# Optimization experiments

Hardware: AMD Instinct MI355X
Metric: run time of the kernel (lower is better)

## Reference

```python
import jax, jax.numpy as jnp
import numpy as np

N_USER = 100000
N_ITEM = 50000
N_NODES = N_USER + N_ITEM
EMB = 64
NNZ = 4000000
BATCH = 4096
N_LAYERS = 3  # len(eval(args.layer_size)) with layer_size=[64,64,64]


def setup_inputs() -> dict:
    key = jax.random.key(0)
    k = jax.random.split(key, 8)
    adj_rows = jax.random.randint(k[0], (NNZ,), 0, N_NODES, dtype=jnp.int32)
    adj_cols = jax.random.randint(k[1], (NNZ,), 0, N_NODES, dtype=jnp.int32)
    adj_vals = jax.random.uniform(k[2], (NNZ,), dtype=jnp.float32)
    user_emb = jax.random.normal(k[3], (N_USER, EMB), dtype=jnp.float32)
    item_emb = jax.random.normal(k[4], (N_ITEM, EMB), dtype=jnp.float32)
    users = jax.random.randint(k[5], (BATCH,), 0, N_USER, dtype=jnp.int32)
    pos_items = jax.random.randint(k[6], (BATCH,), 0, N_ITEM, dtype=jnp.int32)
    neg_items = jax.random.randint(k[7], (BATCH,), 0, N_ITEM, dtype=jnp.int32)
    return {
        "adj_rows": adj_rows, "adj_cols": adj_cols, "adj_vals": adj_vals,
        "user_emb": user_emb, "item_emb": item_emb,
        "users": users, "pos_items": pos_items, "neg_items": neg_items,
    }


def _spmm(rows, cols, vals, x):
    # sparse [N,N] @ dense [N,D] via gather + segment-sum (COO)
    gathered = vals[:, None] * x[cols]          # [nnz, D]
    return jax.ops.segment_sum(gathered, rows, num_segments=N_NODES)


def reference(adj_rows, adj_cols, adj_vals, user_emb, item_emb,
              users, pos_items, neg_items):
    ego = jnp.concatenate([user_emb, item_emb], axis=0)  # [N, D]
    # Source quirk: ego_embeddings is never updated in the layer loop, so
    # every layer appends the same A_hat @ ego; mean over [ego] + L copies.
    prop = _spmm(adj_rows, adj_cols, adj_vals, ego)      # [N, D]
    light_out = (ego + N_LAYERS * prop) / (N_LAYERS + 1)
    u_g = light_out[:N_USER]
    i_g = light_out[N_USER:]
    out = jnp.stack([u_g[users], i_g[pos_items], i_g[neg_items]], axis=0)
    return out  # [3, BATCH, EMB]
```

## Files before the change

kernel.cpp:

```cpp
#include <hip/hip_runtime.h>

#define N_USER 100000
#define N_ITEM 50000
#define N_NODES 150000
#define EMB 64
#define NNZ 4000000
#define BATCH 4096
#define NSLOTS (3 * BATCH)
#define CAP 128

#define BM_OFF   0
#define CUR_OFF  19200
#define CT_OFF   68352
#define PROP_OFF 668416
#define BKT_OFF  3814144

__global__ void mark_kernel(const int* __restrict__ users,
                            const int* __restrict__ pos_items,
                            const int* __restrict__ neg_items,
                            unsigned int* __restrict__ bitmask,
                            int* __restrict__ ctab) {
    int t = blockIdx.x * blockDim.x + threadIdx.x;
    int k = t >> 12;
    int i = t & 4095;
    int node;
    if (k == 0)      node = users[i];
    else if (k == 1) node = N_USER + pos_items[i];
    else             node = N_USER + neg_items[i];
    atomicOr(bitmask + (node >> 5), 1u << (node & 31));
    atomicCAS(ctab + node, -1, t);
}

__global__ void scatter_kernel(const int* __restrict__ rows,
                               const int* __restrict__ cols,
                               const float* __restrict__ vals,
                               const unsigned int* __restrict__ bitmask,
                               const int* __restrict__ ctab,
                               unsigned int* __restrict__ cursor,
                               uint2* __restrict__ bucket) {
    int tid = blockIdx.x * blockDim.x + threadIdx.x;
    int row = rows[tid];
    int col = cols[tid];
    float val = vals[tid];
    unsigned int w = bitmask[row >> 5];
    if ((w >> (row & 31)) & 1) {
        int cid = ctab[row];
        unsigned int pos = atomicAdd(cursor + cid, 1u);
        if (pos < CAP)
            bucket[(size_t)cid * CAP + pos] =
                make_uint2((unsigned int)col, __float_as_uint(val));
    }
}

__global__ void accum_kernel(const unsigned int* __restrict__ cursor,
                             const uint2* __restrict__ bucket,
                             const float* __restrict__ user_emb,
                             const float* __restrict__ item_emb,
                             float* __restrict__ prop) {
    int t = blockIdx.x * blockDim.x + threadIdx.x;
    int wv = t >> 6;
    int lane = t & 63;
    unsigned int n = cursor[wv];
    if (n > CAP) n = CAP;
    const uint2* bkt = bucket + (size_t)wv * CAP;
    float acc = 0.0f;
    for (unsigned int base = 0; base < n; base += 8) {
        #pragma unroll
        for (int u = 0; u < 8; u++) {
            unsigned int e = base + (unsigned int)u;
            uint2 ev = bkt[e < n ? e : n - 1];
            int c = (int)ev.x;
            float v = __uint_as_float(ev.y);
            const float* x = (c < N_USER) ? user_emb + (size_t)c * EMB
                                          : item_emb + (size_t)(c - N_USER) * EMB;
            float xv = x[lane];
            acc += (e < n) ? v * xv : 0.0f;
        }
    }
    prop[(size_t)wv * EMB + lane] = acc;
}

__global__ void gather_kernel(const int* __restrict__ users,
                              const int* __restrict__ pos_items,
                              const int* __restrict__ neg_items,
                              const float* __restrict__ user_emb,
                              const float* __restrict__ item_emb,
                              const int* __restrict__ ctab,
                              const float* __restrict__ prop,
                              float* __restrict__ out) {
    int t = blockIdx.x * blockDim.x + threadIdx.x;
    int slot = t >> 4;
    int sub = t & 15;
    int k = slot >> 12;
    int i = slot & 4095;
    int node;
    if (k == 0)      node = users[i];
    else if (k == 1) node = N_USER + pos_items[i];
    else             node = N_USER + neg_items[i];
    const float4* ego = (const float4*)((node < N_USER)
                          ? user_emb + (size_t)node * EMB
                          : item_emb + (size_t)(node - N_USER) * EMB);
    float4 e = ego[sub];
    int cid = ctab[node];
    float4 p = ((const float4*)(prop + (size_t)cid * EMB))[sub];
    float4 o;
    o.x = (e.x + 3.0f * p.x) * 0.25f;
    o.y = (e.y + 3.0f * p.y) * 0.25f;
    o.z = (e.z + 3.0f * p.z) * 0.25f;
    o.w = (e.w + 3.0f * p.w) * 0.25f;
    ((float4*)out)[t] = o;
}

extern "C" void kernel_launch(void* const* d_in, const int* in_sizes, int n_in,
                              void* d_out, int out_size, void* d_ws, size_t ws_size,
                              hipStream_t stream) {
    const int*   adj_rows = (const int*)  d_in[0];
    const int*   adj_cols = (const int*)  d_in[1];
    const float* adj_vals = (const float*)d_in[2];
    const float* user_emb = (const float*)d_in[3];
    const float* item_emb = (const float*)d_in[4];
    const int*   users    = (const int*)  d_in[5];
    const int*   pos      = (const int*)  d_in[6];
    const int*   neg      = (const int*)  d_in[7];
    float* out = (float*)d_out;

    unsigned int* bitmask = (unsigned int*)((char*)d_ws + BM_OFF);
    unsigned int* cursor  = (unsigned int*)((char*)d_ws + CUR_OFF);
    int*          ctab    = (int*)         ((char*)d_ws + CT_OFF);
    float*        prop    = (float*)       ((char*)d_ws + PROP_OFF);
    uint2*        bucket  = (uint2*)       ((char*)d_ws + BKT_OFF);

    hipMemsetAsync((char*)d_ws + BM_OFF, 0, CT_OFF, stream);
    hipMemsetAsync((char*)d_ws + CT_OFF, 0xFF, N_NODES * 4, stream);

    mark_kernel<<<48, 256, 0, stream>>>(users, pos, neg, bitmask, ctab);

    scatter_kernel<<<15625, 256, 0, stream>>>(adj_rows, adj_cols, adj_vals,
                                              bitmask, ctab, cursor, bucket);

    accum_kernel<<<3072, 256, 0, stream>>>(cursor, bucket, user_emb, item_emb, prop);

    gather_kernel<<<768, 256, 0, stream>>>(users, pos, neg,
                                           user_emb, item_emb, ctab, prop, out);
}
```

Baseline: 171.8 us.

## Fuse accumulation into output gather, vectorize edge scan, drop ctab memset

The per-node accumulation is merged into the final gather kernel, so the intermediate prop buffer and one launch disappear. Each wave loads eight bucket entries cooperatively and broadcasts them with lane shuffles. The edge scatter now reads rows, cols and vals as 4-wide vectors, one thread per four edges. The ctab initialisation memset is removed by having mark_kernel do plain racing stores. In exchange, duplicate batch slots now each recompute their node's accumulation, and ctab entries for unmarked nodes keep stale values, which are never read.

Result: slower. 179.3 us (+4.4%).

```diff
diff --git a/kernel.cpp b/kernel.cpp
--- a/kernel.cpp
+++ b/kernel.cpp
@@ -12,8 +12,7 @@
 #define BM_OFF   0
 #define CUR_OFF  19200
 #define CT_OFF   68352
-#define PROP_OFF 668416
-#define BKT_OFF  3814144
+#define BKT_OFF  668416
 
 __global__ void mark_kernel(const int* __restrict__ users,
                             const int* __restrict__ pos_items,
@@ -28,87 +27,79 @@
     else if (k == 1) node = N_USER + pos_items[i];
     else             node = N_USER + neg_items[i];
     atomicOr(bitmask + (node >> 5), 1u << (node & 31));
-    atomicCAS(ctab + node, -1, t);
+    ctab[node] = t;
 }
 
-__global__ void scatter_kernel(const int* __restrict__ rows,
-                               const int* __restrict__ cols,
-                               const float* __restrict__ vals,
+#define E4 (NNZ / 4)
+__global__ void scatter_kernel(const int4* __restrict__ rows4,
+                               const int4* __restrict__ cols4,
+                               const float4* __restrict__ vals4,
                                const unsigned int* __restrict__ bitmask,
                                const int* __restrict__ ctab,
                                unsigned int* __restrict__ cursor,
                                uint2* __restrict__ bucket) {
-    int tid = blockIdx.x * blockDim.x + threadIdx.x;
-    int row = rows[tid];
-    int col = cols[tid];
-    float val = vals[tid];
-    unsigned int w = bitmask[row >> 5];
-    if ((w >> (row & 31)) & 1) {
-        int cid = ctab[row];
-        unsigned int pos = atomicAdd(cursor + cid, 1u);
-        if (pos < CAP)
-            bucket[(size_t)cid * CAP + pos] =
-                make_uint2((unsigned int)col, __float_as_uint(val));
+    int t = blockIdx.x * blockDim.x + threadIdx.x;
+    if (t >= E4) return;
+    int4   r4 = rows4[t];
+    int4   c4 = cols4[t];
+    float4 v4 = vals4[t];
+    int    rs[4] = {r4.x, r4.y, r4.z, r4.w};
+    int    cs[4] = {c4.x, c4.y, c4.z, c4.w};
+    float  vs[4] = {v4.x, v4.y, v4.z, v4.w};
+    #pragma unroll
+    for (int u = 0; u < 4; u++) {
+        int row = rs[u];
+        if ((bitmask[row >> 5] >> (row & 31)) & 1) {
+            int cid = ctab[row];
+            unsigned int pos = atomicAdd(cursor + cid, 1u);
+            if (pos < CAP)
+                bucket[(size_t)cid * CAP + pos] =
+                    make_uint2((unsigned int)cs[u], __float_as_uint(vs[u]));
+        }
     }
 }
 
-__global__ void accum_kernel(const unsigned int* __restrict__ cursor,
-                             const uint2* __restrict__ bucket,
-                             const float* __restrict__ user_emb,
-                             const float* __restrict__ item_emb,
-                             float* __restrict__ prop) {
+__global__ void accum_gather_kernel(const int* __restrict__ users,
+                                    const int* __restrict__ pos_items,
+                                    const int* __restrict__ neg_items,
+                                    const float* __restrict__ user_emb,
+                                    const float* __restrict__ item_emb,
+                                    const int* __restrict__ ctab,
+                                    const unsigned int* __restrict__ cursor,
+                                    const uint2* __restrict__ bucket,
+                                    float* __restrict__ out) {
     int t = blockIdx.x * blockDim.x + threadIdx.x;
-    int wv = t >> 6;
+    int slot = t >> 6;
     int lane = t & 63;
-    unsigned int n = cursor[wv];
-    if (n > CAP) n = CAP;
-    const uint2* bkt = bucket + (size_t)wv * CAP;
-    float acc = 0.0f;
-    for (unsigned int base = 0; base < n; base += 8) {
-        #pragma unroll
-        for (int u = 0; u < 8; u++) {
-            unsigned int e = base + (unsigned int)u;
-            uint2 ev = bkt[e < n ? e : n - 1];
-            int c = (int)ev.x;
-            float v = __uint_as_float(ev.y);
-            const float* x = (c < N_USER) ? user_emb + (size_t)c * EMB
-                                          : item_emb + (size_t)(c - N_USER) * EMB;
-            float xv = x[lane];
-            acc += (e < n) ? v * xv : 0.0f;
-        }
-    }
-    prop[(size_t)wv * EMB + lane] = acc;
-}
-
-__global__ void gather_kernel(const int* __restrict__ users,
-                              const int* __restrict__ pos_items,
-                              const int* __restrict__ neg_items,
-                              const float* __restrict__ user_emb,
-                              const float* __restrict__ item_emb,
-                              const int* __restrict__ ctab,
-                              const float* __restrict__ prop,
-                              float* __restrict__ out) {
-    int t = blockIdx.x * blockDim.x + threadIdx.x;
-    int slot = t >> 4;
-    int sub = t & 15;
     int k = slot >> 12;
     int i = slot & 4095;
     int node;
     if (k == 0)      node = users[i];
     else if (k == 1) node = N_USER + pos_items[i];
     else             node = N_USER + neg_items[i];
-    const float4* ego = (const float4*)((node < N_USER)
-                          ? user_emb + (size_t)node * EMB
-                          : item_emb + (size_t)(node - N_USER) * EMB);
-    float4 e = ego[sub];
+    float ego = (node < N_USER)
+                    ? user_emb[(size_t)node * EMB + lane]
+                    : item_emb[(size_t)(node - N_USER) * EMB + lane];
     int cid = ctab[node];
-    float4 p = ((const float4*)(prop + (size_t)cid * EMB))[sub];
-    float4 o;
-    o.x = (e.x + 3.0f * p.x) * 0.25f;
-    o.y = (e.y + 3.0f * p.y) * 0.25f;
-    o.z = (e.z + 3.0f * p.z) * 0.25f;
-    o.w = (e.w + 3.0f * p.w) * 0.25f;
-    ((float4*)out)[t] = o;
+    unsigned int n = cursor[cid];
+    if (n > CAP) n = CAP;
+    const uint2* bkt = bucket + (size_t)cid * CAP;
+    float acc = 0.0f;
+    for (unsigned int base = 0; base < n; base += 8) {
+        unsigned int e = base + (lane & 7);
+        uint2 ev = bkt[e < n ? e : n - 1];
+        #pragma unroll
+        for (int u = 0; u < 8; u++) {
+            if (base + (unsigned int)u < n) {
+                int   c = __shfl((int)ev.x, u);
+                float v = __int_as_float(__shfl((int)ev.y, u));
+                const float* x = (c < N_USER) ? user_emb + (size_t)c * EMB
+                                              : item_emb + (size_t)(c - N_USER) * EMB;
+                acc += v * x[lane];
+            }
+        }
+    }
+    out[(size_t)slot * EMB + lane] = (ego + 3.0f * acc) * 0.25f;
 }
 
 extern "C" void kernel_launch(void* const* d_in, const int* in_sizes, int n_in,
@@ -127,19 +118,18 @@
     unsigned int* bitmask = (unsigned int*)((char*)d_ws + BM_OFF);
     unsigned int* cursor  = (unsigned int*)((char*)d_ws + CUR_OFF);
     int*          ctab    = (int*)         ((char*)d_ws + CT_OFF);
-    float*        prop    = (float*)       ((char*)d_ws + PROP_OFF);
     uint2*        bucket  = (uint2*)       ((char*)d_ws + BKT_OFF);
 
     hipMemsetAsync((char*)d_ws + BM_OFF, 0, CT_OFF, stream);
-    hipMemsetAsync((char*)d_ws + CT_OFF, 0xFF, N_NODES * 4, stream);
 
     mark_kernel<<<48, 256, 0, stream>>>(users, pos, neg, bitmask, ctab);
 
-    scatter_kernel<<<15625, 256, 0, stream>>>(adj_rows, adj_cols, adj_vals,
-                                              bitmask, ctab, cursor, bucket);
+    scatter_kernel<<<3907, 256, 0, stream>>>((const int4*)adj_rows,
+                                             (const int4*)adj_cols,
+                                             (const float4*)adj_vals,
+                                             bitmask, ctab, cursor, bucket);
 
-    accum_kernel<<<3072, 256, 0, stream>>>(cursor, bucket, user_emb, item_emb, prop);
-
-    gather_kernel<<<768, 256, 0, stream>>>(users, pos, neg,
-                                           user_emb, item_emb, ctab, prop, out);
+    accum_gather_kernel<<<3072, 256, 0, stream>>>(users, pos, neg,
+                                                  user_emb, item_emb,
+                                                  ctab, cursor, bucket, out);
 }
```
